# Kernel optimization log

Hardware: AMD Instinct MI355X
Metric: run time of the kernel (lower is better)

Reference implementation:

```python
import jax, jax.numpy as jnp
import numpy as np

HEADS, DQK, DV = 4, 128, 128
HH, WW = 32, 32
SCALE = DQK ** -0.5
EPS = 1e-5


def bn(x, g, b, m, v):
    # eval-mode BatchNorm2d over channel dim of NCHW
    inv = g * jax.lax.rsqrt(v + EPS)
    return x * inv[:, None, None] + (b - m * inv)[:, None, None]


def rel_to_abs(x):
    # x: (B, Nh, L, 2L-1) -> (B, Nh, L, L)
    B, Nh, L, _ = x.shape
    x = jnp.pad(x, ((0, 0), (0, 0), (0, 0), (0, 1)))
    fx = x.reshape(B, Nh, L * 2 * L)
    fx = jnp.pad(fx, ((0, 0), (0, 0), (0, L - 1)))
    fx = fx.reshape(B, Nh, L + 1, 2 * L - 1)
    return fx[:, :, :L, L - 1:]


def rel_logits_1d(q, rel_k):
    # q: (B, Nh, H, W, D); rel_k: (2W-1, D)
    B, Nh, H, W, D = q.shape
    r = jnp.einsum('bnhwd,rd->bnhwr', q, rel_k)
    r = rel_to_abs(r.reshape(B, Nh * H, W, 2 * W - 1))
    r = r.reshape(B, Nh, H, W, W)
    return jnp.broadcast_to(r[:, :, :, None], (B, Nh, H, H, W, W))


def pos_bias(q, rel_h, rel_w):
    # q: (B, Nh, H*W, D), already scaled
    B, Nh, L, D = q.shape
    q5 = q.reshape(B, Nh, HH, WW, D)
    rw = rel_logits_1d(q5, rel_w)                     # (B,N,H,Hx,W,W)
    rw = rw.transpose(0, 1, 2, 4, 3, 5).reshape(B, Nh, HH * WW, HH * WW)
    rh = rel_logits_1d(q5.transpose(0, 1, 3, 2, 4), rel_h)  # (B,N,W,Wx,H,H)
    rh = rh.transpose(0, 1, 4, 2, 5, 3).reshape(B, Nh, HH * WW, HH * WW)
    return rw + rh


def to_heads(x):
    # (B, Nh*d, H, W) -> (B, Nh, H*W, d)
    B, C, H, W = x.shape
    x = x.reshape(B, HEADS, C // HEADS, H, W)
    return x.transpose(0, 1, 3, 4, 2).reshape(B, HEADS, H * W, C // HEADS)


def mhsa(x, w_qk, w_v, rel_h, rel_w):
    B, C, H, W = x.shape
    qk = jnp.einsum('bchw,oc->bohw', x, w_qk)
    q, k = jnp.split(qk, 2, axis=1)
    v = jnp.einsum('bchw,oc->bohw', x, w_v)
    q, k, v = to_heads(q), to_heads(k), to_heads(v)
    q = q * SCALE
    logits = jnp.einsum('bnid,bnjd->bnij', q, k) + pos_bias(q, rel_h, rel_w)
    weights = jax.nn.softmax(logits, axis=-1)
    out = jnp.einsum('bnij,bnjd->bnid', weights, v)   # (B,Nh,HW,dv)
    out = out.reshape(B, HEADS, H, W, DV).transpose(0, 1, 4, 2, 3)
    return out.reshape(B, HEADS * DV, H, W)


def setup_inputs() -> dict:
    key = jax.random.key(0)
    ks = jax.random.split(key, 12)
    d = {
        'x': jax.random.normal(ks[0], (8, 512, HH, WW), jnp.float32),
        'w_qk': jax.random.normal(ks[1], (2 * HEADS * DQK, 512), jnp.float32) * 0.02,
        'w_v': jax.random.normal(ks[2], (HEADS * DV, 512), jnp.float32) * 0.02,
        'rel_h': jax.random.normal(ks[3], (2 * HH - 1, DQK), jnp.float32) * SCALE,
        'rel_w': jax.random.normal(ks[4], (2 * WW - 1, DQK), jnp.float32) * SCALE,
        'g1': jnp.ones((512,), jnp.float32),
        'b1': jnp.zeros((512,), jnp.float32),
        'm1': jax.random.normal(ks[5], (512,), jnp.float32) * 0.1,
        'v1': jax.random.uniform(ks[6], (512,), jnp.float32) + 0.5,
        'g2': jnp.ones((512,), jnp.float32),
        'b2': jnp.zeros((512,), jnp.float32),
        'm2': jax.random.normal(ks[7], (512,), jnp.float32) * 0.1,
        'v2': jax.random.uniform(ks[8], (512,), jnp.float32) + 0.5,
        'w_fc': jax.random.normal(ks[9], (512, 512, 3, 3), jnp.float32) * 0.02,
        'bias_fc': jnp.zeros((512,), jnp.float32),
    }
    return d


def reference(x, w_qk, w_v, rel_h, rel_w, g1, b1, m1, v1, g2, b2, m2, v2, w_fc, bias_fc):
    out = jax.nn.relu(bn(x, g1, b1, m1, v1))
    out = mhsa(out, w_qk, w_v, rel_h, rel_w)
    x = out + x
    out = jax.nn.relu(bn(x, g2, b2, m2, v2))
    out = jax.lax.conv_general_dilated(
        out, w_fc, window_strides=(1, 1), padding='SAME',
        dimension_numbers=('NCHW', 'OIHW', 'NCHW')) + bias_fc[:, None, None]
    return out + x
```

## Files before the change

kernel.cpp:

```cpp
#include <hip/hip_runtime.h>

typedef __bf16 v8bf __attribute__((ext_vector_type(8)));
typedef float f32x4 __attribute__((ext_vector_type(4)));

#define DEVI static __device__ __forceinline__

DEVI v8bf load8(const __bf16* p) { return *reinterpret_cast<const v8bf*>(p); }

DEVI f32x4 mfma16(v8bf a, v8bf b, f32x4 c) {
  return __builtin_amdgcn_mfma_f32_16x16x32_bf16(a, b, c, 0, 0, 0);
}

DEVI void gld16(const __bf16* g, __bf16* l) {
  __builtin_amdgcn_global_load_lds(
      (const __attribute__((address_space(1))) unsigned int*)(const void*)g,
      (__attribute__((address_space(3))) unsigned int*)(void*)l, 16, 0, 0);
}

#define SCALE_Q 0.08838834764831845f

__global__ void k_cast(const float* __restrict__ src, __bf16* __restrict__ dst, int n) {
  int i = blockIdx.x * 256 + threadIdx.x;
  if (i < n) dst[i] = (__bf16)src[i];
}

__global__ void k_zero(float* __restrict__ p) {
  int i = blockIdx.x * 256 + threadIdx.x;
  f32x4 z = {0.f, 0.f, 0.f, 0.f};
  reinterpret_cast<f32x4*>(p)[i] = z;
}

__global__ void k_repack(const float* __restrict__ wfc, __bf16* __restrict__ Wt) {
  int idx = blockIdx.x * 256 + threadIdx.x;
  const float* src = wfc + (size_t)idx * 9;
#pragma unroll
  for (int tap = 0; tap < 9; ++tap)
    Wt[(size_t)tap * 262144 + idx] = (__bf16)src[tap];
}

__global__ void k_bn1(const float* __restrict__ x, const float* __restrict__ g,
                      const float* __restrict__ bb, const float* __restrict__ m,
                      const float* __restrict__ v, __bf16* __restrict__ y) {
  __shared__ float tile[32][33];
  const int b = blockIdx.z, c0 = blockIdx.y * 32, s0 = blockIdx.x * 32;
  const int tx = threadIdx.x, ty = threadIdx.y;
#pragma unroll
  for (int r = 0; r < 4; ++r) {
    int c = c0 + ty + r * 8;
    float inv = g[c] * rsqrtf(v[c] + 1e-5f);
    float beta = bb[c] - m[c] * inv;
    float val = x[((size_t)b * 512 + c) * 1024 + s0 + tx] * inv + beta;
    tile[ty + r * 8][tx] = fmaxf(val, 0.0f);
  }
  __syncthreads();
#pragma unroll
  for (int r = 0; r < 4; ++r) {
    int s = s0 + ty + r * 8;
    y[((size_t)b * 1024 + s) * 512 + c0 + tx] = (__bf16)tile[tx][ty + r * 8];
  }
}

__global__ void k_bn2(const float* __restrict__ x2, const float* __restrict__ g,
                      const float* __restrict__ bb, const float* __restrict__ m,
                      const float* __restrict__ v, __bf16* __restrict__ zp) {
  __shared__ float tile[32][33];
  const int b = blockIdx.z, c0 = blockIdx.y * 32, s0 = blockIdx.x * 32;
  const int tx = threadIdx.x, ty = threadIdx.y;
#pragma unroll
  for (int r = 0; r < 4; ++r) {
    int c = c0 + ty + r * 8;
    float inv = g[c] * rsqrtf(v[c] + 1e-5f);
    float beta = bb[c] - m[c] * inv;
    float val = x2[((size_t)b * 512 + c) * 1024 + s0 + tx] * inv + beta;
    tile[ty + r * 8][tx] = fmaxf(val, 0.0f);
  }
  __syncthreads();
#pragma unroll
  for (int r = 0; r < 4; ++r) {
    int s = s0 + ty + r * 8;
    int hh = s >> 5, ww = s & 31;
    zp[(((size_t)b * 34 + hh + 1) * 34 + ww + 1) * 512 + c0 + tx] =
        (__bf16)tile[tx][ty + r * 8];
  }
}

__global__ __launch_bounds__(256) void k_proj(
    const __bf16* __restrict__ wall, const __bf16* __restrict__ y,
    __bf16* __restrict__ qout, __bf16* __restrict__ kout,
    __bf16* __restrict__ vout) {
  __shared__ __bf16 As[128 * 32];
  __shared__ __bf16 Bs[128 * 32];
  const int t = threadIdx.x;
  const int wave = t >> 6, lane = t & 63;
  const int l15 = lane & 15, quad = lane >> 4;
  const int mbase = blockIdx.x * 128;
  const int nbase = blockIdx.y * 128;
  const int mh = (wave >> 1) * 64, nh = (wave & 1) * 64;

  const int row0 = t >> 2, part8 = (t & 3) * 8;
  const __bf16* gA0 = wall + (size_t)(mbase + row0) * 512 + part8;
  const __bf16* gA1 = gA0 + (size_t)64 * 512;
  const __bf16* gB0 = y + (size_t)(nbase + row0) * 512 + part8;
  const __bf16* gB1 = gB0 + (size_t)64 * 512;
  __bf16* lA0 = As + (size_t)(wave * 64) * 8;
  __bf16* lA1 = As + (size_t)(256 + wave * 64) * 8;
  __bf16* lB0 = Bs + (size_t)(wave * 64) * 8;
  __bf16* lB1 = Bs + (size_t)(256 + wave * 64) * 8;

  const f32x4 fz = {0.f, 0.f, 0.f, 0.f};
  f32x4 acc[4][4];
#pragma unroll
  for (int i = 0; i < 4; ++i)
#pragma unroll
    for (int j = 0; j < 4; ++j) acc[i][j] = fz;

  for (int k0 = 0; k0 < 512; k0 += 32) {
    __syncthreads();
    gld16(gA0 + k0, lA0);
    gld16(gA1 + k0, lA1);
    gld16(gB0 + k0, lB0);
    gld16(gB1 + k0, lB1);
    __syncthreads();
    v8bf a[4], bfr[4];
#pragma unroll
    for (int i = 0; i < 4; ++i)
      a[i] = load8(&As[(size_t)(mh + i * 16 + l15) * 32 + quad * 8]);
#pragma unroll
    for (int j = 0; j < 4; ++j)
      bfr[j] = load8(&Bs[(size_t)(nh + j * 16 + l15) * 32 + quad * 8]);
#pragma unroll
    for (int i = 0; i < 4; ++i)
#pragma unroll
      for (int j = 0; j < 4; ++j) acc[i][j] = mfma16(a[i], bfr[j], acc[i][j]);
  }

#pragma unroll
  for (int i = 0; i < 4; ++i)
#pragma unroll
    for (int j = 0; j < 4; ++j)
#pragma unroll
      for (int r = 0; r < 4; ++r) {
        int o = mbase + mh + i * 16 + quad * 4 + r;
        int nflat = nbase + nh + j * 16 + l15;
        int b = nflat >> 10, s = nflat & 1023;
        float val = acc[i][j][r];
        if (o < 512) {
          int n = o >> 7, d = o & 127;
          qout[(((size_t)b * 4 + n) * 1024 + s) * 128 + d] = (__bf16)(val * SCALE_Q);
        } else if (o < 1024) {
          int oe = o - 512; int n = oe >> 7, d = oe & 127;
          kout[(((size_t)b * 4 + n) * 1024 + s) * 128 + d] = (__bf16)val;
        } else {
          int oe = o - 1024; int n = oe >> 7, d = oe & 127;
          vout[(((size_t)b * 4 + n) * 128 + d) * 1024 + s] = (__bf16)val;
        }
      }
}

__global__ __launch_bounds__(256, 2) void k_attn(
    const __bf16* __restrict__ q, const __bf16* __restrict__ kmat,
    const __bf16* __restrict__ vt, const __bf16* __restrict__ relh,
    const __bf16* __restrict__ relw, const float* __restrict__ x,
    float* __restrict__ x2) {
  __shared__ __bf16 Ks[4 * 64 * 32];
  __shared__ __bf16 Vs[2 * 128 * 32];
  __shared__ __bf16 P[4 * 16 * 72];
  __shared__ float RWs[64][33];
  __shared__ float RHs[64][33];

  const int Lb = blockIdx.x;
  const int xcd = Lb & 7, local = Lb >> 3;
  const int bn = xcd * 4 + (local & 3);
  const int qblk = local >> 2;
  const int s0 = qblk * 64;

  const int t = threadIdx.x;
  const int wave = t >> 6, lane = t & 63;
  const int l15 = lane & 15, quad = lane >> 4;
  const size_t hoff = ((size_t)bn) << 17;
  const int s0w = s0 + wave * 16;
  const int wlo = (wave & 1) * 16;
  const int h0w = s0w >> 5;

  v8bf aq[4];
  {
    const __bf16* qp = q + hoff + (size_t)(s0w + l15) * 128;
#pragma unroll
    for (int kk = 0; kk < 4; ++kk) aq[kk] = load8(qp + kk * 32 + quad * 8);
  }

#pragma unroll
  for (int nt = 0; nt < 4; ++nt) {
    int rr = nt * 16 + l15;
    const __bf16* bp = relw + (size_t)rr * 128;
    f32x4 acc = {0.f, 0.f, 0.f, 0.f};
#pragma unroll
    for (int kk = 0; kk < 4; ++kk)
      acc = mfma16(aq[kk], load8(bp + kk * 32 + quad * 8), acc);
#pragma unroll
    for (int r = 0; r < 4; ++r) {
      int row = quad * 4 + r;
      int wj = rr + wlo + row - 31;
      if (wj >= 0 && wj < 32) RWs[wave * 16 + row][wj] = acc[r];
    }
  }
#pragma unroll
  for (int nt = 0; nt < 2; ++nt) {
    int hj = nt * 16 + l15;
    const __bf16* bp = relh + (size_t)(hj - h0w + 31) * 128;
    f32x4 acc = {0.f, 0.f, 0.f, 0.f};
#pragma unroll
    for (int kk = 0; kk < 4; ++kk)
      acc = mfma16(aq[kk], load8(bp + kk * 32 + quad * 8), acc);
#pragma unroll
    for (int r = 0; r < 4; ++r) RHs[wave * 16 + quad * 4 + r][hj] = acc[r];
  }

  const int row0 = t >> 2, part8 = (t & 3) * 8;
  const __bf16* kg = kmat + hoff + (size_t)row0 * 128 + part8;
  const __bf16* vg = vt + hoff + (size_t)row0 * 1024 + part8;
  __bf16* ksw = Ks + wave * 512;
  __bf16* vsw = Vs + wave * 512;

  const f32x4 fz = {0.f, 0.f, 0.f, 0.f};
  float lsum[4] = {0.f, 0.f, 0.f, 0.f};
  f32x4 oacc[8];
#pragma unroll
  for (int dt = 0; dt < 8; ++dt) oacc[dt] = fz;
  __bf16* Pw = P + wave * 16 * 72;

#pragma unroll 1
  for (int iter = 0; iter < 16; ++iter) {
    const int j0 = iter * 64;
    __syncthreads();
#pragma unroll
    for (int kk = 0; kk < 4; ++kk)
      gld16(kg + (size_t)j0 * 128 + kk * 32, ksw + kk * 2048);
#pragma unroll
    for (int kk2 = 0; kk2 < 2; ++kk2)
#pragma unroll
      for (int dh = 0; dh < 2; ++dh)
        gld16(vg + (size_t)dh * 64 * 1024 + j0 + kk2 * 32,
              vsw + kk2 * 4096 + dh * 2048);
    __syncthreads();

    f32x4 sacc[4];
#pragma unroll
    for (int nj = 0; nj < 4; ++nj) {
      f32x4 a = fz;
#pragma unroll
      for (int kk = 0; kk < 4; ++kk)
        a = mfma16(aq[kk],
                   load8(&Ks[kk * 2048 + (nj * 16 + l15) * 32 + quad * 8]), a);
      sacc[nj] = a;
    }
#pragma unroll
    for (int nj = 0; nj < 4; ++nj) {
      const int wj = (nj & 1) * 16 + l15;
      const int hj = (j0 + nj * 16) >> 5;
#pragma unroll
      for (int r = 0; r < 4; ++r) {
        const int row = quad * 4 + r;
        const int gi = wave * 16 + row;
        float val = sacc[nj][r] + RWs[gi][wj] + RHs[gi][hj];
        float p = __expf(fminf(val, 60.0f));
        lsum[r] += p;
        Pw[row * 72 + nj * 16 + l15] = (__bf16)p;
      }
    }
    v8bf pf[2];
#pragma unroll
    for (int kk2 = 0; kk2 < 2; ++kk2)
      pf[kk2] = *reinterpret_cast<const v8bf*>(&Pw[l15 * 72 + kk2 * 32 + quad * 8]);
#pragma unroll
    for (int dt = 0; dt < 8; ++dt) {
      f32x4 a = oacc[dt];
#pragma unroll
      for (int kk2 = 0; kk2 < 2; ++kk2)
        a = mfma16(pf[kk2],
                   load8(&Vs[kk2 * 4096 + (dt * 16 + l15) * 32 + quad * 8]), a);
      oacc[dt] = a;
    }
  }

#pragma unroll
  for (int r = 0; r < 4; ++r)
#pragma unroll
    for (int msk = 8; msk >= 1; msk >>= 1) lsum[r] += __shfl_xor(lsum[r], msk);

#pragma unroll
  for (int r = 0; r < 4; ++r) {
    float inv = 1.0f / lsum[r];
    int s = s0w + quad * 4 + r;
#pragma unroll
    for (int dt = 0; dt < 8; ++dt) {
      int d = dt * 16 + l15;
      size_t idx = ((size_t)bn * 128 + d) * 1024 + s;
      x2[idx] = oacc[dt][r] * inv + x[idx];
    }
  }
}

__global__ __launch_bounds__(256) void k_conv(
    const __bf16* __restrict__ Wt, const __bf16* __restrict__ zp,
    const float* __restrict__ bias, const float* __restrict__ x2,
    float* __restrict__ out) {
  __shared__ __bf16 As[4 * 128 * 32];
  __shared__ __bf16 Bs[4 * 128 * 32];
  const int t = threadIdx.x;
  const int wave = t >> 6, lane = t & 63;
  const int l15 = lane & 15, quad = lane >> 4;
  const int mbase = blockIdx.x * 128;
  const int nbase = blockIdx.y * 128;
  const int mh = (wave >> 1) * 64, nh = (wave & 1) * 64;

  const int row0 = t >> 2;
  const int part8 = (t & 3) * 8;
  const __bf16* gA0 = Wt + (size_t)(mbase + row0) * 512 + part8;
  const __bf16* gA1 = gA0 + (size_t)64 * 512;
  const int n0 = nbase + row0;
  const int b0 = n0 >> 10, sp = n0 & 1023;
  const __bf16* gB0 =
      zp + ((size_t)(b0 * 34 + (sp >> 5) + 1) * 34 + (sp & 31) + 1) * 512 + part8;
  const __bf16* gB1 = gB0 + (size_t)2 * 34 * 512;
  const int wofs = wave * 512;

  const f32x4 fz = {0.f, 0.f, 0.f, 0.f};
  f32x4 acc[4][4];
#pragma unroll
  for (int i = 0; i < 4; ++i)
#pragma unroll
    for (int j = 0; j < 4; ++j) acc[i][j] = fz;

#pragma unroll 1
  for (int tap = 0; tap < 9; ++tap) {
    const int dh = tap / 3 - 1, dw = tap % 3 - 1;
    const size_t aoff = (size_t)tap * 512 * 512;
    const int boff = (dh * 34 + dw) * 512;
#pragma unroll 1
    for (int k0 = 0; k0 < 512; k0 += 128) {
      __syncthreads();
#pragma unroll
      for (int c = 0; c < 4; ++c) {
        const int kq = k0 + c * 32;
        gld16(gA0 + aoff + kq, As + c * 4096 + wofs);
        gld16(gA1 + aoff + kq, As + c * 4096 + 2048 + wofs);
        gld16(gB0 + boff + kq, Bs + c * 4096 + wofs);
        gld16(gB1 + boff + kq, Bs + c * 4096 + 2048 + wofs);
      }
      __syncthreads();
#pragma unroll
      for (int c = 0; c < 4; ++c) {
        v8bf a[4], bfr[4];
#pragma unroll
        for (int i = 0; i < 4; ++i)
          a[i] = load8(&As[c * 4096 + (mh + i * 16 + l15) * 32 + quad * 8]);
#pragma unroll
        for (int j = 0; j < 4; ++j)
          bfr[j] = load8(&Bs[c * 4096 + (nh + j * 16 + l15) * 32 + quad * 8]);
#pragma unroll
        for (int i = 0; i < 4; ++i)
#pragma unroll
          for (int j = 0; j < 4; ++j) acc[i][j] = mfma16(a[i], bfr[j], acc[i][j]);
      }
    }
  }

#pragma unroll
  for (int i = 0; i < 4; ++i)
#pragma unroll
    for (int j = 0; j < 4; ++j)
#pragma unroll
      for (int r = 0; r < 4; ++r) {
        int o = mbase + mh + i * 16 + quad * 4 + r;
        int nn = nbase + nh + j * 16 + l15;
        int bb2 = nn >> 10, s = nn & 1023;
        size_t idx = ((size_t)bb2 * 512 + o) * 1024 + s;
        out[idx] = acc[i][j][r] + bias[o] + x2[idx];
      }
}

extern "C" void kernel_launch(void* const* d_in, const int* in_sizes, int n_in,
                              void* d_out, int out_size, void* d_ws, size_t ws_size,
                              hipStream_t stream) {
  const float* x    = (const float*)d_in[0];
  const float* wqk  = (const float*)d_in[1];
  const float* wv   = (const float*)d_in[2];
  const float* relh = (const float*)d_in[3];
  const float* relw = (const float*)d_in[4];
  const float* g1   = (const float*)d_in[5];
  const float* b1   = (const float*)d_in[6];
  const float* m1   = (const float*)d_in[7];
  const float* v1   = (const float*)d_in[8];
  const float* g2   = (const float*)d_in[9];
  const float* b2   = (const float*)d_in[10];
  const float* m2   = (const float*)d_in[11];
  const float* v2   = (const float*)d_in[12];
  const float* wfc  = (const float*)d_in[13];
  const float* bfc  = (const float*)d_in[14];
  float* out = (float*)d_out;

  char* p = (char*)d_ws;
  __bf16* y    = (__bf16*)p; p += (size_t)8 * 1024 * 512 * 2;
  __bf16* qb   = (__bf16*)p; p += (size_t)8 * 4 * 1024 * 128 * 2;
  __bf16* kb   = (__bf16*)p; p += (size_t)8 * 4 * 1024 * 128 * 2;
  __bf16* vb   = (__bf16*)p; p += (size_t)8 * 4 * 1024 * 128 * 2;
  __bf16* Wt   = (__bf16*)p; p += (size_t)9 * 512 * 512 * 2;
  __bf16* wqkb = (__bf16*)p; p += (size_t)1024 * 512 * 2;
  __bf16* wvb  = (__bf16*)p; p += (size_t)512 * 512 * 2;
  __bf16* rhb  = (__bf16*)p; p += 32768;
  __bf16* rwb  = (__bf16*)p; p += 32768;
  float*  x2   = (float*)p;  p += (size_t)8 * 512 * 1024 * 4;
  __bf16* zpad = (__bf16*)p; p += (size_t)8 * 34 * 34 * 512 * 2;

  k_cast<<<dim3((1024 * 512 + 255) / 256), dim3(256), 0, stream>>>(wqk, wqkb, 1024 * 512);
  k_cast<<<dim3((512 * 512 + 255) / 256), dim3(256), 0, stream>>>(wv, wvb, 512 * 512);
  k_cast<<<dim3((63 * 128 + 255) / 256), dim3(256), 0, stream>>>(relh, rhb, 63 * 128);
  k_cast<<<dim3((63 * 128 + 255) / 256), dim3(256), 0, stream>>>(relw, rwb, 63 * 128);
  k_repack<<<dim3(512 * 512 / 256), dim3(256), 0, stream>>>(wfc, Wt);
  k_zero<<<dim3(591872 / 256), dim3(256), 0, stream>>>((float*)zpad);
  k_bn1<<<dim3(32, 16, 8), dim3(32, 8), 0, stream>>>(x, g1, b1, m1, v1, y);
  k_proj<<<dim3(12, 64), dim3(256), 0, stream>>>(wqkb, y, qb, kb, vb);
  k_attn<<<dim3(512), dim3(256), 0, stream>>>(qb, kb, vb, rhb, rwb, x, x2);
  k_bn2<<<dim3(32, 16, 8), dim3(32, 8), 0, stream>>>(x2, g2, b2, m2, v2, zpad);
  k_conv<<<dim3(4, 64, 1), dim3(256), 0, stream>>>(Wt, zpad, bfc, x2, out);
}
```

Measured before the change: 269.9 us.

## Split conv reduction dimension in two and merge prep kernels into one launch

The 3x3 conv GEMM now splits its input channels into two halves, which doubles the grid from 256 to 512 blocks. Each block writes fp32 partial sums to a scratch buffer that reuses the dead y/q/k/v workspace. A new k_sum kernel adds the two partials, the bias and the residual. Separately, the four cast kernels, the weight repack and the zero-fill are merged into one k_prep launch to cut launch count. The split improves CU fill and occupancy, at the cost of about 32MB of extra partial-sum writes and reads plus one more kernel.

Result: faster. 241.6 us (-10.5%).

```diff
diff --git a/kernel.cpp b/kernel.cpp
--- a/kernel.cpp
+++ b/kernel.cpp
@@ -19,23 +19,36 @@
 
 #define SCALE_Q 0.08838834764831845f
 
-__global__ void k_cast(const float* __restrict__ src, __bf16* __restrict__ dst, int n) {
-  int i = blockIdx.x * 256 + threadIdx.x;
-  if (i < n) dst[i] = (__bf16)src[i];
-}
-
-__global__ void k_zero(float* __restrict__ p) {
-  int i = blockIdx.x * 256 + threadIdx.x;
-  f32x4 z = {0.f, 0.f, 0.f, 0.f};
-  reinterpret_cast<f32x4*>(p)[i] = z;
-}
-
-__global__ void k_repack(const float* __restrict__ wfc, __bf16* __restrict__ Wt) {
-  int idx = blockIdx.x * 256 + threadIdx.x;
-  const float* src = wfc + (size_t)idx * 9;
-#pragma unroll
-  for (int tap = 0; tap < 9; ++tap)
-    Wt[(size_t)tap * 262144 + idx] = (__bf16)src[tap];
+__global__ void k_prep(const float* __restrict__ wqk, const float* __restrict__ wv,
+                       const float* __restrict__ relh, const float* __restrict__ relw,
+                       const float* __restrict__ wfc, __bf16* __restrict__ wqkb,
+                       __bf16* __restrict__ wvb, __bf16* __restrict__ rhb,
+                       __bf16* __restrict__ rwb, __bf16* __restrict__ Wt,
+                       float* __restrict__ zpad4) {
+  const int bid = blockIdx.x, tid = threadIdx.x;
+  if (bid < 2048) {
+    int i = bid * 256 + tid;
+    wqkb[i] = (__bf16)wqk[i];
+  } else if (bid < 3072) {
+    int i = (bid - 2048) * 256 + tid;
+    wvb[i] = (__bf16)wv[i];
+  } else if (bid < 3104) {
+    int i = (bid - 3072) * 256 + tid;
+    if (i < 8064) rhb[i] = (__bf16)relh[i];
+  } else if (bid < 3136) {
+    int i = (bid - 3104) * 256 + tid;
+    if (i < 8064) rwb[i] = (__bf16)relw[i];
+  } else if (bid < 4160) {
+    int i = (bid - 3136) * 256 + tid;
+    const float* src = wfc + (size_t)i * 9;
+#pragma unroll
+    for (int tap = 0; tap < 9; ++tap)
+      Wt[(size_t)tap * 262144 + i] = (__bf16)src[tap];
+  } else {
+    int i = (bid - 4160) * 256 + tid;
+    f32x4 z = {0.f, 0.f, 0.f, 0.f};
+    reinterpret_cast<f32x4*>(zpad4)[i] = z;
+  }
 }
 
 __global__ void k_bn1(const float* __restrict__ x, const float* __restrict__ g,
@@ -301,27 +314,32 @@
   }
 }
 
-__global__ __launch_bounds__(256) void k_conv(
+__global__ __launch_bounds__(256, 2) void k_conv(
     const __bf16* __restrict__ Wt, const __bf16* __restrict__ zp,
-    const float* __restrict__ bias, const float* __restrict__ x2,
-    float* __restrict__ out) {
+    float* __restrict__ part) {
   __shared__ __bf16 As[4 * 128 * 32];
   __shared__ __bf16 Bs[4 * 128 * 32];
   const int t = threadIdx.x;
   const int wave = t >> 6, lane = t & 63;
   const int l15 = lane & 15, quad = lane >> 4;
-  const int mbase = blockIdx.x * 128;
-  const int nbase = blockIdx.y * 128;
+
+  const int id = blockIdx.x;
+  const int combo = id & 7;
+  const int ot = combo >> 1, sp = combo & 1;
+  const int nt = id >> 3;
+  const int mbase = ot * 128;
+  const int nbase = nt * 128;
+  const int cs = sp * 256;
   const int mh = (wave >> 1) * 64, nh = (wave & 1) * 64;
 
   const int row0 = t >> 2;
   const int part8 = (t & 3) * 8;
-  const __bf16* gA0 = Wt + (size_t)(mbase + row0) * 512 + part8;
+  const __bf16* gA0 = Wt + (size_t)(mbase + row0) * 512 + cs + part8;
   const __bf16* gA1 = gA0 + (size_t)64 * 512;
   const int n0 = nbase + row0;
-  const int b0 = n0 >> 10, sp = n0 & 1023;
+  const int b0 = n0 >> 10, spn = n0 & 1023;
   const __bf16* gB0 =
-      zp + ((size_t)(b0 * 34 + (sp >> 5) + 1) * 34 + (sp & 31) + 1) * 512 + part8;
+      zp + ((size_t)(b0 * 34 + (spn >> 5) + 1) * 34 + (spn & 31) + 1) * 512 + cs + part8;
   const __bf16* gB1 = gB0 + (size_t)2 * 34 * 512;
   const int wofs = wave * 512;
 
@@ -338,7 +356,7 @@
     const size_t aoff = (size_t)tap * 512 * 512;
     const int boff = (dh * 34 + dw) * 512;
 #pragma unroll 1
-    for (int k0 = 0; k0 < 512; k0 += 128) {
+    for (int k0 = 0; k0 < 256; k0 += 128) {
       __syncthreads();
 #pragma unroll
       for (int c = 0; c < 4; ++c) {
@@ -366,6 +384,7 @@
     }
   }
 
+  float* pout = part + (size_t)sp * 8 * 512 * 1024;
 #pragma unroll
   for (int i = 0; i < 4; ++i)
 #pragma unroll
@@ -375,9 +394,22 @@
         int o = mbase + mh + i * 16 + quad * 4 + r;
         int nn = nbase + nh + j * 16 + l15;
         int bb2 = nn >> 10, s = nn & 1023;
-        size_t idx = ((size_t)bb2 * 512 + o) * 1024 + s;
-        out[idx] = acc[i][j][r] + bias[o] + x2[idx];
+        pout[((size_t)bb2 * 512 + o) * 1024 + s] = acc[i][j][r];
       }
+}
+
+__global__ void k_sum(const float* __restrict__ part, const float* __restrict__ bias,
+                      const float* __restrict__ x2, float* __restrict__ out) {
+  int i = blockIdx.x * 256 + threadIdx.x;
+  int o = (i >> 8) & 511;
+  f32x4 p0 = reinterpret_cast<const f32x4*>(part)[i];
+  f32x4 p1 = reinterpret_cast<const f32x4*>(part + (size_t)8 * 512 * 1024)[i];
+  f32x4 xr = reinterpret_cast<const f32x4*>(x2)[i];
+  float bo = bias[o];
+  f32x4 r;
+#pragma unroll
+  for (int c = 0; c < 4; ++c) r[c] = p0[c] + p1[c] + bo + xr[c];
+  reinterpret_cast<f32x4*>(out)[i] = r;
 }
 
 extern "C" void kernel_launch(void* const* d_in, const int* in_sizes, int n_in,
@@ -412,16 +444,14 @@
   __bf16* rwb  = (__bf16*)p; p += 32768;
   float*  x2   = (float*)p;  p += (size_t)8 * 512 * 1024 * 4;
   __bf16* zpad = (__bf16*)p; p += (size_t)8 * 34 * 34 * 512 * 2;
-
-  k_cast<<<dim3((1024 * 512 + 255) / 256), dim3(256), 0, stream>>>(wqk, wqkb, 1024 * 512);
-  k_cast<<<dim3((512 * 512 + 255) / 256), dim3(256), 0, stream>>>(wv, wvb, 512 * 512);
-  k_cast<<<dim3((63 * 128 + 255) / 256), dim3(256), 0, stream>>>(relh, rhb, 63 * 128);
-  k_cast<<<dim3((63 * 128 + 255) / 256), dim3(256), 0, stream>>>(relw, rwb, 63 * 128);
-  k_repack<<<dim3(512 * 512 / 256), dim3(256), 0, stream>>>(wfc, Wt);
-  k_zero<<<dim3(591872 / 256), dim3(256), 0, stream>>>((float*)zpad);
+  float* part = (float*)d_ws;
+
+  k_prep<<<dim3(6472), dim3(256), 0, stream>>>(wqk, wv, relh, relw, wfc,
+                                               wqkb, wvb, rhb, rwb, Wt, (float*)zpad);
   k_bn1<<<dim3(32, 16, 8), dim3(32, 8), 0, stream>>>(x, g1, b1, m1, v1, y);
   k_proj<<<dim3(12, 64), dim3(256), 0, stream>>>(wqkb, y, qb, kb, vb);
   k_attn<<<dim3(512), dim3(256), 0, stream>>>(qb, kb, vb, rhb, rwb, x, x2);
   k_bn2<<<dim3(32, 16, 8), dim3(32, 8), 0, stream>>>(x2, g2, b2, m2, v2, zpad);
-  k_conv<<<dim3(4, 64, 1), dim3(256), 0, stream>>>(Wt, zpad, bfc, x2, out);
-}
+  k_conv<<<dim3(512), dim3(256), 0, stream>>>(Wt, zpad, part);
+  k_sum<<<dim3(4096), dim3(256), 0, stream>>>(part, bfc, x2, out);
+}
```
